# Kernel tuning notes

Hardware: AMD Instinct MI355X
Metric: run time of the kernel (lower is better)

The kernel has to match this reference:

```python
import jax, jax.numpy as jnp
import numpy as np
import math

N = 50000      # nodes
E = 800000     # edges
F_IN = 64      # input node features
H = 4          # heads
C = 32         # hidden_channels (per-head dim)
HC = H * C     # 128
ED = 4         # edge_dim
G = 1000       # graphs in batch


def _lin(key, fin, fout, bias=True):
    k1, k2 = jax.random.split(key)
    w = jax.random.normal(k1, (fin, fout), jnp.float32) * (1.0 / math.sqrt(fin))
    if bias:
        b = jax.random.normal(k2, (fout,), jnp.float32) * 0.02
        return w, b
    return w


def setup_inputs() -> dict:
    key = jax.random.key(0)
    ks = jax.random.split(key, 24)
    x = jax.random.normal(ks[0], (N, F_IN), jnp.float32)
    edge_index = jax.random.randint(ks[1], (2, E), 0, N)
    edge_attr = jax.random.normal(ks[2], (E, ED), jnp.float32)
    batch = jnp.sort(jax.random.randint(ks[3], (N,), 0, G))
    inp = {"x": x, "edge_index": edge_index, "edge_attr": edge_attr, "batch": batch}
    fins = [F_IN, HC, HC]
    i = 4
    for l in range(3):
        fin = fins[l]
        inp[f"wq{l+1}"], inp[f"bq{l+1}"] = _lin(ks[i], fin, HC); i += 1
        inp[f"wk{l+1}"], inp[f"bk{l+1}"] = _lin(ks[i], fin, HC); i += 1
        inp[f"wv{l+1}"], inp[f"bv{l+1}"] = _lin(ks[i], fin, HC); i += 1
        inp[f"we{l+1}"] = _lin(ks[i], ED, HC, bias=False); i += 1
        inp[f"ws{l+1}"], inp[f"bs{l+1}"] = _lin(ks[i], fin, HC); i += 1
    inp["wlin"], inp["blin"] = _lin(ks[i], HC, 1)
    return inp


def _segment_softmax(alpha, seg, n):
    # numerically-stable softmax over edges grouped by destination node
    m = jax.ops.segment_max(alpha, seg, num_segments=n)
    m = jnp.where(jnp.isfinite(m), m, 0.0)
    a = jnp.exp(alpha - m[seg])
    s = jax.ops.segment_sum(a, seg, num_segments=n)
    return a / (s[seg] + 1e-16)


def _conv(x, src, dst, ea, wq, bq, wk, bk, wv, bv, we, ws, bs):
    # PyG TransformerConv (concat=True, root_weight=True, beta=False)
    n = x.shape[0]
    q = (x @ wq + bq).reshape(n, H, C)
    k = (x @ wk + bk).reshape(n, H, C)
    v = (x @ wv + bv).reshape(n, H, C)
    e = (ea @ we).reshape(-1, H, C)          # [E,H,C] edge projection
    kj = k[src] + e                           # key of source + edge
    alpha = jnp.einsum('ehc,ehc->eh', q[dst], kj) / math.sqrt(C)  # [E,H]
    alpha = _segment_softmax(alpha, dst, n)
    msg = (v[src] + e) * alpha[..., None]     # [E,H,C]
    out = jax.ops.segment_sum(msg, dst, num_segments=n).reshape(n, HC)
    return out + x @ ws + bs                  # skip connection


def reference(x, edge_index, edge_attr, batch,
              wq1, bq1, wk1, bk1, wv1, bv1, we1, ws1, bs1,
              wq2, bq2, wk2, bk2, wv2, bv2, we2, ws2, bs2,
              wq3, bq3, wk3, bk3, wv3, bv3, we3, ws3, bs3,
              wlin, blin):
    src, dst = edge_index[0], edge_index[1]
    h = jax.nn.relu(_conv(x, src, dst, edge_attr, wq1, bq1, wk1, bk1, wv1, bv1, we1, ws1, bs1))
    h = jax.nn.relu(_conv(h, src, dst, edge_attr, wq2, bq2, wk2, bk2, wv2, bv2, we2, ws2, bs2))
    h = _conv(h, src, dst, edge_attr, wq3, bq3, wk3, bk3, wv3, bv3, we3, ws3, bs3)
    # global_mean_pool
    s = jax.ops.segment_sum(h, batch, num_segments=G)
    cnt = jax.ops.segment_sum(jnp.ones((h.shape[0],), h.dtype), batch, num_segments=G)
    pooled = s / jnp.maximum(cnt, 1.0)[:, None]
    # dropout is identity in eval mode
    return pooled @ wlin + blin
```

## Files before the change

### kernel.cpp

```cpp
#include <hip/hip_runtime.h>
#include <math.h>

#define NN 50000
#define EE 800000
#define GG 1000

typedef __attribute__((ext_vector_type(2))) _Float16 h2f;
typedef __attribute__((ext_vector_type(4))) _Float16 h4f;
typedef __attribute__((ext_vector_type(8))) _Float16 h8f;
typedef __attribute__((ext_vector_type(4))) float f32x4;

#if __has_builtin(__builtin_amdgcn_fdot2)
#define FDOT2(a, b, c) __builtin_amdgcn_fdot2((a), (b), (c), false)
#else
#define FDOT2(a, b, c) ((float)(a)[0] * (float)(b)[0] + (float)(a)[1] * (float)(b)[1] + (c))
#endif

static inline int ceil_div(int a, int b) { return (a + b - 1) / b; }

union EU { int2 i; h4f h; };


__global__ __launch_bounds__(256) void hist_k(const int* __restrict__ ei, int* __restrict__ cnt)
{
    int e = blockIdx.x * 256 + threadIdx.x;
    if (e >= EE) return;
    atomicAdd(&cnt[ei[EE + e]], 1);
}

__global__ __launch_bounds__(1024) void scan1_k(const int* __restrict__ cnt, int n,
                                                int* __restrict__ rowptr, int* __restrict__ bsum,
                                                const int* __restrict__ batch,
                                                int* __restrict__ gptr)
{
    __shared__ int tmp[1024];
    const int tid = threadIdx.x;
    const int i = blockIdx.x * 1024 + tid;
    tmp[tid] = (i < n) ? cnt[i] : 0;
    __syncthreads();
    for (int off = 1; off < 1024; off <<= 1) {
        int t = (tid >= off) ? tmp[tid - off] : 0;
        __syncthreads();
        tmp[tid] += t;
        __syncthreads();
    }
    if (i < n) rowptr[i + 1] = tmp[tid];
    if (tid == 1023) bsum[blockIdx.x] = tmp[1023];
    if (i < NN) {
        int b = batch[i];
        int bp = (i == 0) ? -1 : batch[i - 1];
        for (int g = bp + 1; g <= b; ++g) gptr[g] = i;
        if (i == NN - 1) for (int g = b + 1; g <= GG; ++g) gptr[g] = NN;
    }
}

__global__ __launch_bounds__(1024) void scan3_k(int* __restrict__ rowptr,
                                                int* __restrict__ wcur,
                                                const int* __restrict__ bsum, int n)
{
    __shared__ int base_s;
    const int tid = threadIdx.x;
    if (tid < 64) {
        int v = (tid < (int)blockIdx.x) ? bsum[tid] : 0;
#pragma unroll
        for (int off = 1; off < 64; off <<= 1) v += __shfl_xor(v, off);
        if (tid == 0) base_s = v;
    }
    __syncthreads();
    const int base = base_s;
    int i = blockIdx.x * 1024 + tid;
    if (i < n) {
        int v = rowptr[i + 1] + base;
        rowptr[i + 1] = v;
        if (i + 1 < n) wcur[i + 1] = v;
    }
    if (i == 0) { rowptr[0] = 0; wcur[0] = 0; }
}

__global__ __launch_bounds__(256) void scatter_k(const int* __restrict__ ei,
                                                 const float4* __restrict__ ea,
                                                 int* __restrict__ wcur,
                                                 int4* __restrict__ edges)
{
    int e = blockIdx.x * 256 + threadIdx.x;
    if (e >= EE) return;
    int dst = ei[EE + e];
    int pos = atomicAdd(&wcur[dst], 1);
    float4 a = ea[e];
    EU u; u.h = h4f{(_Float16)a.x, (_Float16)a.y, (_Float16)a.z, (_Float16)a.w};
    edges[pos] = make_int4(ei[e], u.i.x, u.i.y, 0);
}

struct W12 { const float* w[12]; };

__global__ __launch_bounds__(64) void shuffle_w12(W12 ws, _Float16* __restrict__ out)
{
    const int m = blockIdx.y;
    const int K = (m < 4) ? 64 : 128;
    const int nblk = (K / 16) * 8;
    if (blockIdx.x >= nblk) return;
    const int s = blockIdx.x >> 3, c16 = blockIdx.x & 7;
    const int lane = threadIdx.x;
    const float* __restrict__ w = ws.w[m];
    const int kbase = s * 16 + (lane >> 4) * 4;
    const int col = c16 * 16 + (lane & 15);
    h4f h;
#pragma unroll
    for (int j = 0; j < 4; ++j) h[j] = (_Float16)w[(size_t)(kbase + j) * 128 + col];
    size_t base = (m < 4) ? (size_t)m * 64 * 128
                          : (size_t)4 * 64 * 128 + (size_t)(m - 4) * 128 * 128;
    reinterpret_cast<h4f*>(out + base)[(size_t)blockIdx.x * 64 + lane] = h;
}

template<int K, bool F32IN>
__global__ __launch_bounds__(256) void gemm_mfma(
    const void* __restrict__ xin, const _Float16* __restrict__ wshuf,
    const float* __restrict__ bq, const float* __restrict__ bk,
    const float* __restrict__ bv, const float* __restrict__ bs,
    _Float16* __restrict__ qout, _Float16* __restrict__ kout,
    _Float16* __restrict__ vout, _Float16* __restrict__ skout)
{
    constexpr int KS = K / 16;
    constexpr int PADK = K + 8;
    __shared__ _Float16 xs[64 * PADK];
    __shared__ _Float16 wt[K * 128];
    const int t = threadIdx.x;
    const int bn = blockIdx.x * 64;
    const int m = blockIdx.y;

    if (F32IN) {
        const float* xf = (const float*)xin;
        constexpr int C4 = K / 4;
        for (int idx = t; idx < 64 * C4; idx += 256) {
            const int row = idx / C4, c4 = idx % C4;
            float4 val = make_float4(0.f, 0.f, 0.f, 0.f);
            if (bn + row < NN)
                val = reinterpret_cast<const float4*>(xf)[(size_t)(bn + row) * C4 + c4];
            h4f h = {(_Float16)val.x, (_Float16)val.y, (_Float16)val.z, (_Float16)val.w};
            *reinterpret_cast<h4f*>(&xs[row * PADK + c4 * 4]) = h;
        }
    } else {
        const _Float16* xh = (const _Float16*)xin;
        constexpr int CH = K / 8;
        for (int idx = t; idx < 64 * CH; idx += 256) {
            const int row = idx / CH, ch = idx % CH;
            h8f val = {0, 0, 0, 0, 0, 0, 0, 0};
            if (bn + row < NN)
                val = reinterpret_cast<const h8f*>(xh + (size_t)(bn + row) * K)[ch];
            *reinterpret_cast<h8f*>(&xs[row * PADK + ch * 8]) = val;
        }
    }
    {
        const h8f* __restrict__ wg = reinterpret_cast<const h8f*>(wshuf + (size_t)m * K * 128);
        h8f* __restrict__ wl8 = reinterpret_cast<h8f*>(wt);
        constexpr int WH8 = K * 16;
        for (int idx = t; idx < WH8; idx += 256) wl8[idx] = wg[idx];
    }
    __syncthreads();

    const int wid = t >> 6, lane = t & 63;
    const int rloc = wid * 16 + (lane & 15);
    const int ko = (lane >> 4) * 4;
    h4f b[KS];
#pragma unroll
    for (int s = 0; s < KS; ++s)
        b[s] = *reinterpret_cast<const h4f*>(&xs[rloc * PADK + s * 16 + ko]);

    const int node = bn + rloc;
    const int hcq = (lane >> 4) * 4;
    const float* bias[4] = {bq, bk, bv, bs};
    _Float16* outs[4] = {qout, kout, vout, skout};
    const h4f* __restrict__ wl = reinterpret_cast<const h4f*>(wt);

    f32x4 acc[8];
#pragma unroll
    for (int c = 0; c < 8; ++c) acc[c] = {0, 0, 0, 0};
#pragma unroll
    for (int c = 0; c < 8; ++c)
#pragma unroll
        for (int s = 0; s < KS; ++s) {
            h4f af = wl[(s * 8 + c) * 64 + lane];
            acc[c] = __builtin_amdgcn_mfma_f32_16x16x16f16(af, b[s], acc[c], 0, 0, 0);
        }
    if (node < NN) {
        const float* bm = bias[m];
        _Float16* dst = outs[m];
#pragma unroll
        for (int c = 0; c < 8; ++c) {
            const int hc = c * 16 + hcq;
            const float4 bb = *reinterpret_cast<const float4*>(&bm[hc]);
            h4f oh = {(_Float16)(acc[c][0] + bb.x), (_Float16)(acc[c][1] + bb.y),
                      (_Float16)(acc[c][2] + bb.z), (_Float16)(acc[c][3] + bb.w)};
            *reinterpret_cast<h4f*>(&dst[(size_t)node * 128 + hc]) = oh;
        }
    }
}

__global__ __launch_bounds__(256, 8) void node_agg(
    const int* __restrict__ rowptr, const int4* __restrict__ edges,
    const _Float16* __restrict__ qh, const _Float16* __restrict__ kh,
    const _Float16* __restrict__ vh, const float* __restrict__ we,
    const _Float16* __restrict__ sk, _Float16* __restrict__ houth, int relu)
{
    __shared__ float we_s[4 * 128];
    const int t = threadIdx.x;
    if (t < 128)
        reinterpret_cast<float4*>(we_s)[t] = reinterpret_cast<const float4*>(we)[t];
    __syncthreads();
    const int node = blockIdx.x * 4 + (t >> 6);
    if (node >= NN) return;
    const int lane = t & 63;
    const int g = lane >> 4, sub = lane & 15, ch0 = sub * 8;
    const int beg = rowptr[node], end = rowptr[node + 1];
    const int deg = end - beg;

    const float sc = 0.17677669529663687f * 1.4426950408889634f;
    const h8f q8 = *reinterpret_cast<const h8f*>(&qh[(size_t)node * 128 + ch0]);
    float qf[8];
#pragma unroll
    for (int j = 0; j < 8; ++j) qf[j] = (float)q8[j] * sc;
    h2f qp[4];
#pragma unroll
    for (int i = 0; i < 4; ++i) {
        qp[i][0] = (_Float16)qf[2 * i];
        qp[i][1] = (_Float16)qf[2 * i + 1];
    }

    float qe[4];
#pragma unroll
    for (int d = 0; d < 4; ++d) {
        const float4 wa = *reinterpret_cast<const float4*>(&we_s[d * 128 + ch0]);
        const float4 wb = *reinterpret_cast<const float4*>(&we_s[d * 128 + ch0 + 4]);
        float pq = wa.x * qf[0] + wa.y * qf[1] + wa.z * qf[2] + wa.w * qf[3]
                 + wb.x * qf[4] + wb.y * qf[5] + wb.z * qf[6] + wb.w * qf[7];
        pq += __shfl_xor(pq, 1); pq += __shfl_xor(pq, 2);
        qe[d] = pq;
    }

    float m = -1e30f, s = 0.f;
    float acc[8] = {0, 0, 0, 0, 0, 0, 0, 0};
    float T[4] = {0, 0, 0, 0};

    const int nt = (deg + 3) >> 2;
    int p = beg + g;
    for (int i = 0; i < nt; ++i, p += 4) {
        const bool act = p < end;
        const int4 r = edges[act ? p : beg];
        const int4 ki = *reinterpret_cast<const int4*>(&kh[(size_t)r.x * 128 + ch0]);
        const int4 vi = *reinterpret_cast<const int4*>(&vh[(size_t)r.x * 128 + ch0]);
        float al = FDOT2(qp[0], __builtin_bit_cast(h2f, ki.x), 0.0f);
        al = FDOT2(qp[1], __builtin_bit_cast(h2f, ki.y), al);
        al = FDOT2(qp[2], __builtin_bit_cast(h2f, ki.z), al);
        al = FDOT2(qp[3], __builtin_bit_cast(h2f, ki.w), al);
        al += __shfl_xor(al, 1); al += __shfl_xor(al, 2);
        const h2f e01 = __builtin_bit_cast(h2f, r.y);
        const h2f e23 = __builtin_bit_cast(h2f, r.z);
        const float f0 = (float)e01[0], f1 = (float)e01[1];
        const float f2 = (float)e23[0], f3 = (float)e23[1];
        al += f0 * qe[0] + f1 * qe[1] + f2 * qe[2] + f3 * qe[3];
        al = act ? al : -1e30f;
        if (__any(al > m + 10.0f)) {
            const float mn = fmaxf(m, al);
            const float rr = exp2f(m - mn);
            s *= rr;
#pragma unroll
            for (int j = 0; j < 8; ++j) acc[j] *= rr;
#pragma unroll
            for (int d = 0; d < 4; ++d) T[d] *= rr;
            m = mn;
        }
        const float pe = exp2f(al - m);
        s += pe;
        const h2f v01 = __builtin_bit_cast(h2f, vi.x);
        const h2f v23 = __builtin_bit_cast(h2f, vi.y);
        const h2f v45 = __builtin_bit_cast(h2f, vi.z);
        const h2f v67 = __builtin_bit_cast(h2f, vi.w);
        acc[0] += pe * (float)v01[0]; acc[1] += pe * (float)v01[1];
        acc[2] += pe * (float)v23[0]; acc[3] += pe * (float)v23[1];
        acc[4] += pe * (float)v45[0]; acc[5] += pe * (float)v45[1];
        acc[6] += pe * (float)v67[0]; acc[7] += pe * (float)v67[1];
        T[0] += pe * f0; T[1] += pe * f1; T[2] += pe * f2; T[3] += pe * f3;
    }

#pragma unroll
    for (int off = 16; off <= 32; off <<= 1) {
        const float mo = __shfl_xor(m, off);
        const float so = __shfl_xor(s, off);
        const float mn = fmaxf(m, mo);
        const float r1 = exp2f(m - mn), r2 = exp2f(mo - mn);
        s = s * r1 + so * r2;
#pragma unroll
        for (int j = 0; j < 8; ++j) {
            const float ao = __shfl_xor(acc[j], off);
            acc[j] = acc[j] * r1 + ao * r2;
        }
#pragma unroll
        for (int d = 0; d < 4; ++d) {
            const float To = __shfl_xor(T[d], off);
            T[d] = T[d] * r1 + To * r2;
        }
        m = mn;
    }

    if (g == 0) {
        const float inv = 1.0f / (s + 1e-16f);
        float4 wa[4], wb[4];
#pragma unroll
        for (int d = 0; d < 4; ++d) {
            wa[d] = *reinterpret_cast<const float4*>(&we_s[d * 128 + ch0]);
            wb[d] = *reinterpret_cast<const float4*>(&we_s[d * 128 + ch0 + 4]);
        }
        const h8f sk8 = *reinterpret_cast<const h8f*>(&sk[(size_t)node * 128 + ch0]);
        float ov[8];
        ov[0] = (acc[0] + wa[0].x * T[0] + wa[1].x * T[1] + wa[2].x * T[2] + wa[3].x * T[3]) * inv + (float)sk8[0];
        ov[1] = (acc[1] + wa[0].y * T[0] + wa[1].y * T[1] + wa[2].y * T[2] + wa[3].y * T[3]) * inv + (float)sk8[1];
        ov[2] = (acc[2] + wa[0].z * T[0] + wa[1].z * T[1] + wa[2].z * T[2] + wa[3].z * T[3]) * inv + (float)sk8[2];
        ov[3] = (acc[3] + wa[0].w * T[0] + wa[1].w * T[1] + wa[2].w * T[2] + wa[3].w * T[3]) * inv + (float)sk8[3];
        ov[4] = (acc[4] + wb[0].x * T[0] + wb[1].x * T[1] + wb[2].x * T[2] + wb[3].x * T[3]) * inv + (float)sk8[4];
        ov[5] = (acc[5] + wb[0].y * T[0] + wb[1].y * T[1] + wb[2].y * T[2] + wb[3].y * T[3]) * inv + (float)sk8[5];
        ov[6] = (acc[6] + wb[0].z * T[0] + wb[1].z * T[1] + wb[2].z * T[2] + wb[3].z * T[3]) * inv + (float)sk8[6];
        ov[7] = (acc[7] + wb[0].w * T[0] + wb[1].w * T[1] + wb[2].w * T[2] + wb[3].w * T[3]) * inv + (float)sk8[7];
        h8f oh;
#pragma unroll
        for (int j = 0; j < 8; ++j) {
            float v = relu ? fmaxf(ov[j], 0.f) : ov[j];
            oh[j] = (_Float16)v;
        }
        *reinterpret_cast<h8f*>(&houth[(size_t)node * 128 + ch0]) = oh;
    }
}


__global__ __launch_bounds__(128) void head_k(
    const _Float16* __restrict__ h, const int* __restrict__ gptr,
    const float* __restrict__ wlin, const float* __restrict__ blin,
    float* __restrict__ out)
{
    __shared__ float red[128];
    const int g = blockIdx.x;
    const int t = threadIdx.x;
    const int beg = gptr[g], end = gptr[g + 1];
    float p = 0.f;
    for (int n = beg; n < end; ++n) p += (float)h[(size_t)n * 128 + t];
    p *= wlin[t];
    red[t] = p;
    __syncthreads();
    for (int off = 64; off; off >>= 1) {
        if (t < off) red[t] += red[t + off];
        __syncthreads();
    }
    if (t == 0) out[g] = red[0] / fmaxf((float)(end - beg), 1.0f) + blin[0];
}

extern "C" void kernel_launch(void* const* d_in, const int* in_sizes, int n_in,
                              void* d_out, int out_size, void* d_ws, size_t ws_size,
                              hipStream_t stream)
{
    const float* x     = (const float*)d_in[0];
    const int*   ei    = (const int*)d_in[1];
    const float* ea    = (const float*)d_in[2];
    const int*   batch = (const int*)d_in[3];
    auto W = [&](int i) { return (const float*)d_in[i]; };

    char* wsb = (char*)d_ws;
    size_t off = 0;
    auto alloc = [&](size_t bytes) { void* p = wsb + off; off += (bytes + 15) & ~15ull; return p; };

    int4*  edges    = (int4*)alloc((size_t)EE * 16);
    _Float16* qh    = (_Float16*)alloc((size_t)NN * 128 * 2);
    _Float16* kh    = (_Float16*)alloc((size_t)NN * 128 * 2);
    _Float16* vh    = (_Float16*)alloc((size_t)NN * 128 * 2);
    _Float16* sk    = (_Float16*)alloc((size_t)NN * 128 * 2);
    _Float16* hh    = (_Float16*)alloc((size_t)NN * 128 * 2);
    _Float16* wshuf = (_Float16*)alloc(((size_t)4 * 64 * 128 + 8 * 128 * 128) * 2);
    int* cnt    = (int*)alloc((size_t)NN * 4);
    int* rowptr = (int*)alloc((size_t)(NN + 1) * 4);
    int* wcur   = (int*)alloc((size_t)NN * 4);
    int* gptr   = (int*)alloc((size_t)(GG + 1) * 4);
    int* bsum   = (int*)alloc((size_t)64 * 4);

    hipMemsetAsync(cnt, 0, NN * sizeof(int), stream);
    hist_k<<<ceil_div(EE, 256), 256, 0, stream>>>(ei, cnt);
    const int NB = ceil_div(NN, 1024);
    scan1_k<<<NB, 1024, 0, stream>>>(cnt, NN, rowptr, bsum, batch, gptr);
    scan3_k<<<NB, 1024, 0, stream>>>(rowptr, wcur, bsum, NN);
    scatter_k<<<ceil_div(EE, 256), 256, 0, stream>>>(ei, (const float4*)ea, wcur, edges);

    W12 w12 = {{ W(4), W(6), W(8), W(11),
                 W(13), W(15), W(17), W(20),
                 W(22), W(24), W(26), W(29) }};
    shuffle_w12<<<dim3(64, 12), 64, 0, stream>>>(w12, wshuf);
    const size_t wsz1 = (size_t)4 * 64 * 128;
    const size_t wsz2 = (size_t)4 * 128 * 128;

    auto layer = [&](int K, const void* xin, const _Float16* wsh, int relu, int wb) {
        dim3 gg(ceil_div(NN, 64), 4);
        if (K == 64)
            gemm_mfma<64, true><<<gg, 256, 0, stream>>>(
                xin, wsh, W(wb + 1), W(wb + 3), W(wb + 5), W(wb + 8), qh, kh, vh, sk);
        else
            gemm_mfma<128, false><<<gg, 256, 0, stream>>>(
                xin, wsh, W(wb + 1), W(wb + 3), W(wb + 5), W(wb + 8), qh, kh, vh, sk);
        node_agg<<<ceil_div(NN, 4), 256, 0, stream>>>(
            rowptr, edges, qh, kh, vh, W(wb + 6), sk, hh, relu);
    };

    layer(64,  x,  wshuf, 1, 4);
    layer(128, hh, wshuf + wsz1, 1, 13);
    layer(128, hh, wshuf + wsz1 + wsz2, 0, 22);

    head_k<<<GG, 128, 0, stream>>>(hh, gptr, W(31), W(32), (float*)d_out);
}
```

Baseline: 417.7 us.

## Fuse CSR build and weight shuffle into one cooperative kernel

Replaces the memset, histogram, two scan kernels, scatter kernel and weight-shuffle kernel with a single cooperative-groups kernel that uses grid-wide syncs between phases. The goal is to remove several kernel launch overheads and inter-kernel gaps in the preprocessing stage. In exchange, grid.sync barriers add their own cost, the fixed 1024-block grid must be co-resident on the device, and the scan now works in 256-element chunks with a second single-block scan.

```diff
diff --git a/kernel.cpp b/kernel.cpp
--- a/kernel.cpp
+++ b/kernel.cpp
@@ -1,5 +1,8 @@
 #include <hip/hip_runtime.h>
+#include <hip/hip_cooperative_groups.h>
 #include <math.h>
+
+namespace cg = cooperative_groups;
 
 #define NN 50000
 #define EE 800000
@@ -20,96 +23,97 @@
 
 union EU { int2 i; h4f h; };
 
-
-__global__ __launch_bounds__(256) void hist_k(const int* __restrict__ ei, int* __restrict__ cnt)
+struct W12 { const float* w[12]; };
+
+__global__ __launch_bounds__(256) void csr_coop(
+    const int* __restrict__ ei, const float4* __restrict__ ea,
+    const int* __restrict__ batch, W12 ws,
+    int* __restrict__ cnt, int* __restrict__ rowptr, int* __restrict__ wcur,
+    int* __restrict__ csum, int4* __restrict__ edges, int* __restrict__ gptr,
+    _Float16* __restrict__ wshuf)
 {
-    int e = blockIdx.x * 256 + threadIdx.x;
-    if (e >= EE) return;
-    atomicAdd(&cnt[ei[EE + e]], 1);
-}
-
-__global__ __launch_bounds__(1024) void scan1_k(const int* __restrict__ cnt, int n,
-                                                int* __restrict__ rowptr, int* __restrict__ bsum,
-                                                const int* __restrict__ batch,
-                                                int* __restrict__ gptr)
-{
-    __shared__ int tmp[1024];
-    const int tid = threadIdx.x;
-    const int i = blockIdx.x * 1024 + tid;
-    tmp[tid] = (i < n) ? cnt[i] : 0;
-    __syncthreads();
-    for (int off = 1; off < 1024; off <<= 1) {
-        int t = (tid >= off) ? tmp[tid - off] : 0;
-        __syncthreads();
-        tmp[tid] += t;
-        __syncthreads();
-    }
-    if (i < n) rowptr[i + 1] = tmp[tid];
-    if (tid == 1023) bsum[blockIdx.x] = tmp[1023];
-    if (i < NN) {
+    cg::grid_group grid = cg::this_grid();
+    __shared__ int tmp[256];
+    const int tid = blockIdx.x * 256 + threadIdx.x;
+    const int NT = gridDim.x * 256;
+    const int NCH = (NN + 255) / 256;
+
+    for (int i = tid; i < NN; i += NT) cnt[i] = 0;
+    for (int i = tid; i < NN; i += NT) {
         int b = batch[i];
         int bp = (i == 0) ? -1 : batch[i - 1];
         for (int g = bp + 1; g <= b; ++g) gptr[g] = i;
         if (i == NN - 1) for (int g = b + 1; g <= GG; ++g) gptr[g] = NN;
     }
-}
-
-__global__ __launch_bounds__(1024) void scan3_k(int* __restrict__ rowptr,
-                                                int* __restrict__ wcur,
-                                                const int* __restrict__ bsum, int n)
-{
-    __shared__ int base_s;
-    const int tid = threadIdx.x;
-    if (tid < 64) {
-        int v = (tid < (int)blockIdx.x) ? bsum[tid] : 0;
-#pragma unroll
-        for (int off = 1; off < 64; off <<= 1) v += __shfl_xor(v, off);
-        if (tid == 0) base_s = v;
-    }
-    __syncthreads();
-    const int base = base_s;
-    int i = blockIdx.x * 1024 + tid;
-    if (i < n) {
-        int v = rowptr[i + 1] + base;
+    for (int it = tid; it < 12 * 64 * 64; it += NT) {
+        const int m = it / (64 * 64);
+        const int rem = it % (64 * 64);
+        const int blkx = rem / 64, lane = rem % 64;
+        const int K = (m < 4) ? 64 : 128;
+        const int nblk = (K / 16) * 8;
+        if (blkx < nblk) {
+            const int s = blkx >> 3, c16 = blkx & 7;
+            const float* __restrict__ w = ws.w[m];
+            const int kbase = s * 16 + (lane >> 4) * 4;
+            const int col = c16 * 16 + (lane & 15);
+            h4f h;
+#pragma unroll
+            for (int j = 0; j < 4; ++j) h[j] = (_Float16)w[(size_t)(kbase + j) * 128 + col];
+            size_t base = (m < 4) ? (size_t)m * 64 * 128
+                                  : (size_t)4 * 64 * 128 + (size_t)(m - 4) * 128 * 128;
+            reinterpret_cast<h4f*>(wshuf + base)[(size_t)blkx * 64 + lane] = h;
+        }
+    }
+    grid.sync();
+
+    for (int e = tid; e < EE; e += NT) atomicAdd(&cnt[ei[EE + e]], 1);
+    grid.sync();
+
+    for (int ch = blockIdx.x; ch < NCH; ch += gridDim.x) {
+        const int i = ch * 256 + threadIdx.x;
+        tmp[threadIdx.x] = (i < NN) ? cnt[i] : 0;
+        __syncthreads();
+        for (int off = 1; off < 256; off <<= 1) {
+            int t2 = (threadIdx.x >= off) ? tmp[threadIdx.x - off] : 0;
+            __syncthreads();
+            tmp[threadIdx.x] += t2;
+            __syncthreads();
+        }
+        if (i < NN) rowptr[i + 1] = tmp[threadIdx.x];
+        if (threadIdx.x == 255) csum[ch] = tmp[255];
+        __syncthreads();
+    }
+    grid.sync();
+
+    if (blockIdx.x == 0) {
+        const int v = (threadIdx.x < NCH) ? csum[threadIdx.x] : 0;
+        tmp[threadIdx.x] = v;
+        __syncthreads();
+        for (int off = 1; off < 256; off <<= 1) {
+            int t2 = (threadIdx.x >= off) ? tmp[threadIdx.x - off] : 0;
+            __syncthreads();
+            tmp[threadIdx.x] += t2;
+            __syncthreads();
+        }
+        if (threadIdx.x < NCH) csum[threadIdx.x] = tmp[threadIdx.x] - v;
+    }
+    grid.sync();
+
+    for (int i = tid; i < NN; i += NT) {
+        const int v = rowptr[i + 1] + csum[i >> 8];
         rowptr[i + 1] = v;
-        if (i + 1 < n) wcur[i + 1] = v;
-    }
-    if (i == 0) { rowptr[0] = 0; wcur[0] = 0; }
-}
-
-__global__ __launch_bounds__(256) void scatter_k(const int* __restrict__ ei,
-                                                 const float4* __restrict__ ea,
-                                                 int* __restrict__ wcur,
-                                                 int4* __restrict__ edges)
-{
-    int e = blockIdx.x * 256 + threadIdx.x;
-    if (e >= EE) return;
-    int dst = ei[EE + e];
-    int pos = atomicAdd(&wcur[dst], 1);
-    float4 a = ea[e];
-    EU u; u.h = h4f{(_Float16)a.x, (_Float16)a.y, (_Float16)a.z, (_Float16)a.w};
-    edges[pos] = make_int4(ei[e], u.i.x, u.i.y, 0);
-}
-
-struct W12 { const float* w[12]; };
-
-__global__ __launch_bounds__(64) void shuffle_w12(W12 ws, _Float16* __restrict__ out)
-{
-    const int m = blockIdx.y;
-    const int K = (m < 4) ? 64 : 128;
-    const int nblk = (K / 16) * 8;
-    if (blockIdx.x >= nblk) return;
-    const int s = blockIdx.x >> 3, c16 = blockIdx.x & 7;
-    const int lane = threadIdx.x;
-    const float* __restrict__ w = ws.w[m];
-    const int kbase = s * 16 + (lane >> 4) * 4;
-    const int col = c16 * 16 + (lane & 15);
-    h4f h;
-#pragma unroll
-    for (int j = 0; j < 4; ++j) h[j] = (_Float16)w[(size_t)(kbase + j) * 128 + col];
-    size_t base = (m < 4) ? (size_t)m * 64 * 128
-                          : (size_t)4 * 64 * 128 + (size_t)(m - 4) * 128 * 128;
-    reinterpret_cast<h4f*>(out + base)[(size_t)blockIdx.x * 64 + lane] = h;
+        if (i + 1 < NN) wcur[i + 1] = v;
+    }
+    if (tid == 0) { rowptr[0] = 0; wcur[0] = 0; }
+    grid.sync();
+
+    for (int e = tid; e < EE; e += NT) {
+        const int dst = ei[EE + e];
+        const int pos = atomicAdd(&wcur[dst], 1);
+        const float4 a = ea[e];
+        EU u; u.h = h4f{(_Float16)a.x, (_Float16)a.y, (_Float16)a.z, (_Float16)a.w};
+        edges[pos] = make_int4(ei[e], u.i.x, u.i.y, 0);
+    }
 }
 
 template<int K, bool F32IN>
@@ -377,19 +381,20 @@
     int* rowptr = (int*)alloc((size_t)(NN + 1) * 4);
     int* wcur   = (int*)alloc((size_t)NN * 4);
     int* gptr   = (int*)alloc((size_t)(GG + 1) * 4);
-    int* bsum   = (int*)alloc((size_t)64 * 4);
-
-    hipMemsetAsync(cnt, 0, NN * sizeof(int), stream);
-    hist_k<<<ceil_div(EE, 256), 256, 0, stream>>>(ei, cnt);
-    const int NB = ceil_div(NN, 1024);
-    scan1_k<<<NB, 1024, 0, stream>>>(cnt, NN, rowptr, bsum, batch, gptr);
-    scan3_k<<<NB, 1024, 0, stream>>>(rowptr, wcur, bsum, NN);
-    scatter_k<<<ceil_div(EE, 256), 256, 0, stream>>>(ei, (const float4*)ea, wcur, edges);
+    int* csum   = (int*)alloc((size_t)256 * 4);
 
     W12 w12 = {{ W(4), W(6), W(8), W(11),
                  W(13), W(15), W(17), W(20),
                  W(22), W(24), W(26), W(29) }};
-    shuffle_w12<<<dim3(64, 12), 64, 0, stream>>>(w12, wshuf);
+    {
+        const float4* ea4 = (const float4*)ea;
+        void* args[] = { (void*)&ei, (void*)&ea4, (void*)&batch, (void*)&w12,
+                         (void*)&cnt, (void*)&rowptr, (void*)&wcur, (void*)&csum,
+                         (void*)&edges, (void*)&gptr, (void*)&wshuf };
+        (void)hipLaunchCooperativeKernel((const void*)csr_coop, dim3(1024), dim3(256),
+                                         args, 0, stream);
+    }
+
     const size_t wsz1 = (size_t)4 * 64 * 128;
     const size_t wsz2 = (size_t)4 * 128 * 128;
 
```

New measurement: 898.5 us. 115% more time.
